# Optimization experiments

Hardware: AMD Instinct MI355X
Metric: run time of the kernel (lower is better)

The kernel has to match this reference:

```python
import jax, jax.numpy as jnp
import numpy as np

BETA = 0.1
CODEBOOK_SIZE = 32768
EMBED_DIM = 4


def setup_inputs() -> dict:
    key = jax.random.key(0)
    kx, ke = jax.random.split(key)
    x = jax.random.normal(kx, (1, 2, EMBED_DIM, 64, 64), dtype=jnp.float32)
    # codebook init mirrors uniform(-1/K, 1/K) but scale doesn't affect correctness;
    # use normal scaled small to keep distances well-conditioned
    E = jax.random.uniform(ke, (CODEBOOK_SIZE, EMBED_DIM), dtype=jnp.float32,
                           minval=-1.0 / CODEBOOK_SIZE, maxval=1.0 / CODEBOOK_SIZE)
    return {"x": x, "E": E}


def reference(x, E):
    b, t, c, h, w = x.shape
    # (B,T,C,H,W) -> (N, C) with N = B*T*H*W
    x_flat = jnp.transpose(x, (0, 1, 3, 4, 2)).reshape(-1, c)
    d = (jnp.sum(x_flat * x_flat, axis=1, keepdims=True)
         + jnp.sum(E * E, axis=1)
         - 2.0 * jnp.einsum('nc,kc->nk', x_flat, E))
    codes = jnp.argmin(d, axis=1)                      # (N,)
    z_q = E[codes].reshape(b, t, h, w, c)              # gather
    z_q = jnp.transpose(z_q, (0, 1, 4, 2, 3))          # (B,T,C,H,W)
    # commitment + codebook loss
    qloss = (jnp.mean((jax.lax.stop_gradient(z_q) - x) ** 2)
             + BETA * jnp.mean((z_q - jax.lax.stop_gradient(x)) ** 2))
    # straight-through estimator
    z_q_st = x + jax.lax.stop_gradient(z_q - x)
    codes = codes.reshape(b, t, h, w)
    return z_q_st, qloss, codes
```

## Files before the change

kernel.cpp:

```cpp
#include <hip/hip_runtime.h>
#include <cfloat>

#define KC    32768
#define NPTS  8192
#define TPB   256
#define PPT   8
#define PTS_PER_BLK (TPB * PPT)
#define NPB   (NPTS / PTS_PER_BLK)
#define NC    256
#define CHUNK (KC / NC)

typedef float v2f __attribute__((ext_vector_type(2)));

__device__ __forceinline__ v2f pk_fma(v2f a, v2f b, v2f c) {
    v2f d; asm("v_pk_fma_f32 %0, %1, %2, %3" : "=v"(d) : "v"(a), "v"(b), "v"(c)); return d;
}
__device__ __forceinline__ v2f pk_add(v2f a, v2f b) {
    v2f d; asm("v_pk_add_f32 %0, %1, %2" : "=v"(d) : "v"(a), "v"(b)); return d;
}
template<int H>
__device__ __forceinline__ v2f pk_mul_s(v2f a, v2f b) {
    v2f d;
    if constexpr (H == 0)
        asm("v_pk_mul_f32 %0, %1, %2 op_sel:[0,0] op_sel_hi:[0,1]" : "=v"(d) : "v"(a), "v"(b));
    else
        asm("v_pk_mul_f32 %0, %1, %2 op_sel:[1,0] op_sel_hi:[1,1]" : "=v"(d) : "v"(a), "v"(b));
    return d;
}
template<int H>
__device__ __forceinline__ v2f pk_fma_s(v2f a, v2f b, v2f c) {
    v2f d;
    if constexpr (H == 0)
        asm("v_pk_fma_f32 %0, %1, %2, %3 op_sel:[0,0,0] op_sel_hi:[0,1,1]" : "=v"(d) : "v"(a), "v"(b), "v"(c));
    else
        asm("v_pk_fma_f32 %0, %1, %2, %3 op_sel:[1,0,0] op_sel_hi:[1,1,1]" : "=v"(d) : "v"(a), "v"(b), "v"(c));
    return d;
}
__device__ __forceinline__ float min3f(float a, float b, float c) {
    float d; asm("v_min3_f32 %0, %1, %2, %3" : "=v"(d) : "v"(a), "v"(b), "v"(c)); return d;
}

__global__ __launch_bounds__(TPB) void k_dist(const float* __restrict__ x,
                                              const float* __restrict__ E,
                                              float* __restrict__ dmn) {
#pragma clang fp contract(off)
    __shared__ __align__(16) float lds[5 * CHUNK];
    float* exL = lds;
    float* eyL = lds + CHUNK;
    float* ezL = lds + 2 * CHUNK;
    float* ewL = lds + 3 * CHUNK;
    float* bL  = lds + 4 * CHUNK;

    const int chunk = blockIdx.x;
    const int pblk  = blockIdx.y;
    const int tid   = threadIdx.x;
    const int kbase = chunk * CHUNK;

    for (int i = tid; i < CHUNK; i += TPB) {
        float4 e = ((const float4*)E)[kbase + i];
        exL[i] = e.x; eyL[i] = e.y; ezL[i] = e.z; ewL[i] = e.w;
        bL[i]  = ((e.x * e.x + e.y * e.y) + e.z * e.z) + e.w * e.w;
    }
    __syncthreads();

    v2f X01[PPT], X23[PPT], Av[PPT];
#pragma unroll
    for (int i = 0; i < PPT; ++i) {
        const int p  = pblk * PTS_PER_BLK + i * TPB + tid;
        const int t  = p >> 12, s = p & 4095;
        const int xb = t * 16384 + s;
        const float x0 = x[xb];
        const float x1 = x[xb + 4096];
        const float x2 = x[xb + 8192];
        const float x3 = x[xb + 12288];
        X01[i] = v2f{x0, x1};
        X23[i] = v2f{x2, x3};
        const float a = ((x0 * x0 + x1 * x1) + x2 * x2) + x3 * x3;
        Av[i] = v2f{a, a};
    }
    const v2f M2 = {-2.0f, -2.0f};

    float bd[PPT];
#pragma unroll
    for (int i = 0; i < PPT; ++i) bd[i] = FLT_MAX;

#pragma unroll 2
    for (int q = 0; q < CHUNK / 4; ++q) {
        float4 vx = *(const float4*)(exL + 4 * q);
        float4 vy = *(const float4*)(eyL + 4 * q);
        float4 vz = *(const float4*)(ezL + 4 * q);
        float4 vw = *(const float4*)(ewL + 4 * q);
        float4 vb = *(const float4*)(bL  + 4 * q);

        const v2f ex0 = {vx.x, vx.y}, ex1 = {vx.z, vx.w};
        const v2f ey0 = {vy.x, vy.y}, ey1 = {vy.z, vy.w};
        const v2f ez0 = {vz.x, vz.y}, ez1 = {vz.z, vz.w};
        const v2f ew0 = {vw.x, vw.y}, ew1 = {vw.z, vw.w};
        const v2f b0  = {vb.x, vb.y}, b1  = {vb.z, vb.w};

#pragma unroll
        for (int i = 0; i < PPT; ++i) {
            v2f m0 = pk_fma_s<1>(X23[i], ew0, pk_fma_s<0>(X23[i], ez0,
                      pk_fma_s<1>(X01[i], ey0, pk_mul_s<0>(X01[i], ex0))));
            v2f m1 = pk_fma_s<1>(X23[i], ew1, pk_fma_s<0>(X23[i], ez1,
                      pk_fma_s<1>(X01[i], ey1, pk_mul_s<0>(X01[i], ex1))));
            v2f d0 = pk_fma(M2, m0, pk_add(Av[i], b0));
            v2f d1 = pk_fma(M2, m1, pk_add(Av[i], b1));
            bd[i] = min3f(min3f(bd[i], d0.x, d0.y), d1.x, d1.y);
        }
    }
#pragma unroll
    for (int i = 0; i < PPT; ++i) {
        const int p = pblk * PTS_PER_BLK + i * TPB + tid;
        dmn[chunk * NPTS + p] = bd[i];
    }
}

__global__ __launch_bounds__(256) void k_merge(const float* __restrict__ x,
                                               const float* __restrict__ E,
                                               const float* __restrict__ dmn,
                                               float* __restrict__ out,
                                               double* __restrict__ partials) {
#pragma clang fp contract(off)
    const int tid  = threadIdx.x;
    const int sub  = tid & 7;
    const int pidx = tid >> 3;
    const int p    = blockIdx.x * 32 + pidx;
    const int t    = p >> 12, s = p & 4095;
    const int xb   = t * 16384 + s;

    const float x0 = x[xb];
    const float x1 = x[xb + 4096];
    const float x2 = x[xb + 8192];
    const float x3 = x[xb + 12288];
    const float a  = ((x0 * x0 + x1 * x1) + x2 * x2) + x3 * x3;

    float bd = FLT_MAX;
    int   bc = 0x7fffffff;
#pragma unroll
    for (int i = 0; i < NC / 8; ++i) {
        const int c = sub + 8 * i;
        float d = dmn[c * NPTS + p];
        if (d < bd) { bd = d; bc = c; }
    }
#pragma unroll
    for (int m = 1; m <= 4; m <<= 1) {
        float d2 = __shfl_xor(bd, m);
        int   c2 = __shfl_xor(bc, m);
        if (d2 < bd || (d2 == bd && c2 < bc)) { bd = d2; bc = c2; }
    }

    const int kb = bc * CHUNK;
    int jloc = 1 << 30;
    for (int jj = 0; jj < 16; ++jj) {
        const int j = sub * 16 + jj;
        float4 e = ((const float4*)E)[kb + j];
        float bn = ((e.x * e.x + e.y * e.y) + e.z * e.z) + e.w * e.w;
        float m_ = __builtin_fmaf(x3, e.w, __builtin_fmaf(x2, e.z,
                    __builtin_fmaf(x1, e.y, x0 * e.x)));
        float t_ = a + bn;
        float d_ = __builtin_fmaf(-2.0f, m_, t_);
        if (d_ == bd) jloc = min(jloc, j);
    }
#pragma unroll
    for (int m = 1; m <= 4; m <<= 1) jloc = min(jloc, __shfl_xor(jloc, m));
    const int bk = kb + (jloc & (CHUNK - 1));

    double ls = 0.0;
    if (sub < 4) {
        const int ch  = sub;
        const int idx = xb + ch * 4096;
        float xv   = x[idx];
        float ev   = E[bk * 4 + ch];
        float diff = ev - xv;
        float sq   = diff * diff;
        out[idx]   = xv + diff;
        ls = (double)sq;
        if (ch == 0) out[32769 + p] = (float)bk;
    }
#pragma unroll
    for (int m = 1; m < 64; m <<= 1) ls += __shfl_xor(ls, m);
    __shared__ double sred[4];
    if ((tid & 63) == 0) sred[tid >> 6] = ls;
    __syncthreads();
    if (tid == 0) partials[blockIdx.x] = sred[0] + sred[1] + sred[2] + sred[3];
}

__global__ void k_loss(const double* __restrict__ partials,
                       float* __restrict__ out) {
#pragma clang fp contract(off)
    if (threadIdx.x == 0 && blockIdx.x == 0) {
        double sum = 0.0;
        for (int i = 0; i < 256; ++i) sum += partials[i];
        float mu = (float)(sum * (1.0 / 32768.0));
        float q  = mu + 0.1f * mu;
        out[32768] = q;
    }
}

extern "C" void kernel_launch(void* const* d_in, const int* in_sizes, int n_in,
                              void* d_out, int out_size, void* d_ws, size_t ws_size,
                              hipStream_t stream) {
    const float* x = (const float*)d_in[0];
    const float* E = (const float*)d_in[1];
    float* out = (float*)d_out;

    char* ws = (char*)d_ws;
    double* partials = (double*)ws;
    float*  dmn      = (float*)(ws + 2048);

    dim3 g(NC, NPB);
    k_dist<<<g, TPB, 0, stream>>>(x, E, dmn);
    k_merge<<<NPTS / 32, 256, 0, stream>>>(x, E, dmn, out, partials);
    k_loss<<<1, 64, 0, stream>>>(partials, out);
}
```

Baseline: 50.31 us.

## Stream codebook via scalar loads from precomputed SoA instead of LDS staging

Adds a prep kernel that writes the codebook as structure-of-arrays with precomputed norms. The distance kernel then reads code pairs through wave-uniform scalar loads used directly as packed-FMA scalar operands, instead of staging the chunk in LDS. Points are packed two per vector lane and pre-scaled by -2. This removes LDS reads and a barrier but adds a launch, and it changes the arithmetic order, so minima may not match the merge kernel's exact recompute.

```diff
diff --git a/kernel.cpp b/kernel.cpp
--- a/kernel.cpp
+++ b/kernel.cpp
@@ -12,107 +12,116 @@
 
 typedef float v2f __attribute__((ext_vector_type(2)));
 
-__device__ __forceinline__ v2f pk_fma(v2f a, v2f b, v2f c) {
-    v2f d; asm("v_pk_fma_f32 %0, %1, %2, %3" : "=v"(d) : "v"(a), "v"(b), "v"(c)); return d;
+template<int H> __device__ __forceinline__ v2f pk_mul_sg(double a, v2f b) {
+    v2f d;
+    if constexpr (H == 0)
+        asm("v_pk_mul_f32 %0, %1, %2 op_sel:[0,0] op_sel_hi:[0,1]" : "=v"(d) : "s"(a), "v"(b));
+    else
+        asm("v_pk_mul_f32 %0, %1, %2 op_sel:[1,0] op_sel_hi:[1,1]" : "=v"(d) : "s"(a), "v"(b));
+    return d;
+}
+template<int H> __device__ __forceinline__ v2f pk_fma_sg(double a, v2f b, v2f c) {
+    v2f d;
+    if constexpr (H == 0)
+        asm("v_pk_fma_f32 %0, %1, %2, %3 op_sel:[0,0,0] op_sel_hi:[0,1,1]" : "=v"(d) : "s"(a), "v"(b), "v"(c));
+    else
+        asm("v_pk_fma_f32 %0, %1, %2, %3 op_sel:[1,0,0] op_sel_hi:[1,1,1]" : "=v"(d) : "s"(a), "v"(b), "v"(c));
+    return d;
+}
+template<int H> __device__ __forceinline__ v2f pk_add_sg(double a, v2f b) {
+    v2f d;
+    if constexpr (H == 0)
+        asm("v_pk_add_f32 %0, %1, %2 op_sel:[0,0] op_sel_hi:[0,1]" : "=v"(d) : "s"(a), "v"(b));
+    else
+        asm("v_pk_add_f32 %0, %1, %2 op_sel:[1,0] op_sel_hi:[1,1]" : "=v"(d) : "s"(a), "v"(b));
+    return d;
 }
 __device__ __forceinline__ v2f pk_add(v2f a, v2f b) {
     v2f d; asm("v_pk_add_f32 %0, %1, %2" : "=v"(d) : "v"(a), "v"(b)); return d;
 }
-template<int H>
-__device__ __forceinline__ v2f pk_mul_s(v2f a, v2f b) {
-    v2f d;
-    if constexpr (H == 0)
-        asm("v_pk_mul_f32 %0, %1, %2 op_sel:[0,0] op_sel_hi:[0,1]" : "=v"(d) : "v"(a), "v"(b));
-    else
-        asm("v_pk_mul_f32 %0, %1, %2 op_sel:[1,0] op_sel_hi:[1,1]" : "=v"(d) : "v"(a), "v"(b));
-    return d;
-}
-template<int H>
-__device__ __forceinline__ v2f pk_fma_s(v2f a, v2f b, v2f c) {
-    v2f d;
-    if constexpr (H == 0)
-        asm("v_pk_fma_f32 %0, %1, %2, %3 op_sel:[0,0,0] op_sel_hi:[0,1,1]" : "=v"(d) : "v"(a), "v"(b), "v"(c));
-    else
-        asm("v_pk_fma_f32 %0, %1, %2, %3 op_sel:[1,0,0] op_sel_hi:[1,1,1]" : "=v"(d) : "v"(a), "v"(b), "v"(c));
-    return d;
-}
 __device__ __forceinline__ float min3f(float a, float b, float c) {
     float d; asm("v_min3_f32 %0, %1, %2, %3" : "=v"(d) : "v"(a), "v"(b), "v"(c)); return d;
 }
 
+__global__ __launch_bounds__(256) void k_prep(const float* __restrict__ E,
+                                              float* __restrict__ ec) {
+#pragma clang fp contract(off)
+    const int k = blockIdx.x * 256 + threadIdx.x;
+    float4 e = ((const float4*)E)[k];
+    ec[k]          = e.x;
+    ec[KC + k]     = e.y;
+    ec[2 * KC + k] = e.z;
+    ec[3 * KC + k] = e.w;
+    ec[4 * KC + k] = ((e.x * e.x + e.y * e.y) + e.z * e.z) + e.w * e.w;
+}
+
 __global__ __launch_bounds__(TPB) void k_dist(const float* __restrict__ x,
-                                              const float* __restrict__ E,
+                                              const float* __restrict__ ec,
                                               float* __restrict__ dmn) {
 #pragma clang fp contract(off)
-    __shared__ __align__(16) float lds[5 * CHUNK];
-    float* exL = lds;
-    float* eyL = lds + CHUNK;
-    float* ezL = lds + 2 * CHUNK;
-    float* ewL = lds + 3 * CHUNK;
-    float* bL  = lds + 4 * CHUNK;
+    const double* E0 = (const double*)(ec);
+    const double* E1 = (const double*)(ec + KC);
+    const double* E2 = (const double*)(ec + 2 * KC);
+    const double* E3 = (const double*)(ec + 3 * KC);
+    const double* Bb = (const double*)(ec + 4 * KC);
 
     const int chunk = blockIdx.x;
     const int pblk  = blockIdx.y;
     const int tid   = threadIdx.x;
-    const int kbase = chunk * CHUNK;
-
-    for (int i = tid; i < CHUNK; i += TPB) {
-        float4 e = ((const float4*)E)[kbase + i];
-        exL[i] = e.x; eyL[i] = e.y; ezL[i] = e.z; ewL[i] = e.w;
-        bL[i]  = ((e.x * e.x + e.y * e.y) + e.z * e.z) + e.w * e.w;
-    }
-    __syncthreads();
-
-    v2f X01[PPT], X23[PPT], Av[PPT];
-#pragma unroll
-    for (int i = 0; i < PPT; ++i) {
-        const int p  = pblk * PTS_PER_BLK + i * TPB + tid;
-        const int t  = p >> 12, s = p & 4095;
-        const int xb = t * 16384 + s;
-        const float x0 = x[xb];
-        const float x1 = x[xb + 4096];
-        const float x2 = x[xb + 8192];
-        const float x3 = x[xb + 12288];
-        X01[i] = v2f{x0, x1};
-        X23[i] = v2f{x2, x3};
-        const float a = ((x0 * x0 + x1 * x1) + x2 * x2) + x3 * x3;
-        Av[i] = v2f{a, a};
-    }
-    const v2f M2 = {-2.0f, -2.0f};
-
-    float bd[PPT];
-#pragma unroll
-    for (int i = 0; i < PPT; ++i) bd[i] = FLT_MAX;
-
-#pragma unroll 2
-    for (int q = 0; q < CHUNK / 4; ++q) {
-        float4 vx = *(const float4*)(exL + 4 * q);
-        float4 vy = *(const float4*)(eyL + 4 * q);
-        float4 vz = *(const float4*)(ezL + 4 * q);
-        float4 vw = *(const float4*)(ewL + 4 * q);
-        float4 vb = *(const float4*)(bL  + 4 * q);
-
-        const v2f ex0 = {vx.x, vx.y}, ex1 = {vx.z, vx.w};
-        const v2f ey0 = {vy.x, vy.y}, ey1 = {vy.z, vy.w};
-        const v2f ez0 = {vz.x, vz.y}, ez1 = {vz.z, vz.w};
-        const v2f ew0 = {vw.x, vw.y}, ew1 = {vw.z, vw.w};
-        const v2f b0  = {vb.x, vb.y}, b1  = {vb.z, vb.w};
-
-#pragma unroll
-        for (int i = 0; i < PPT; ++i) {
-            v2f m0 = pk_fma_s<1>(X23[i], ew0, pk_fma_s<0>(X23[i], ez0,
-                      pk_fma_s<1>(X01[i], ey0, pk_mul_s<0>(X01[i], ex0))));
-            v2f m1 = pk_fma_s<1>(X23[i], ew1, pk_fma_s<0>(X23[i], ez1,
-                      pk_fma_s<1>(X01[i], ey1, pk_mul_s<0>(X01[i], ex1))));
-            v2f d0 = pk_fma(M2, m0, pk_add(Av[i], b0));
-            v2f d1 = pk_fma(M2, m1, pk_add(Av[i], b1));
-            bd[i] = min3f(min3f(bd[i], d0.x, d0.y), d1.x, d1.y);
+    const int kb2   = chunk * (CHUNK / 2);
+
+    v2f Xm0[4], Xm1[4], Xm2[4], Xm3[4], Aab[4];
+#pragma unroll
+    for (int u = 0; u < 4; ++u) {
+        float xs[2][4], aa[2];
+#pragma unroll
+        for (int h = 0; h < 2; ++h) {
+            const int i = 2 * u + h;
+            const int p = pblk * PTS_PER_BLK + i * TPB + tid;
+            const int t = p >> 12, s = p & 4095;
+            const int xb = t * 16384 + s;
+            const float x0 = x[xb], x1 = x[xb + 4096], x2 = x[xb + 8192], x3 = x[xb + 12288];
+            xs[h][0] = x0; xs[h][1] = x1; xs[h][2] = x2; xs[h][3] = x3;
+            aa[h] = ((x0 * x0 + x1 * x1) + x2 * x2) + x3 * x3;
         }
-    }
-#pragma unroll
-    for (int i = 0; i < PPT; ++i) {
-        const int p = pblk * PTS_PER_BLK + i * TPB + tid;
-        dmn[chunk * NPTS + p] = bd[i];
+        Xm0[u] = v2f{-2.0f * xs[0][0], -2.0f * xs[1][0]};
+        Xm1[u] = v2f{-2.0f * xs[0][1], -2.0f * xs[1][1]};
+        Xm2[u] = v2f{-2.0f * xs[0][2], -2.0f * xs[1][2]};
+        Xm3[u] = v2f{-2.0f * xs[0][3], -2.0f * xs[1][3]};
+        Aab[u] = v2f{aa[0], aa[1]};
+    }
+
+    float bdA[4], bdB[4];
+#pragma unroll
+    for (int u = 0; u < 4; ++u) { bdA[u] = FLT_MAX; bdB[u] = FLT_MAX; }
+
+#pragma unroll 4
+    for (int q = 0; q < CHUNK / 2; ++q) {
+        const double se0 = E0[kb2 + q];
+        const double se1 = E1[kb2 + q];
+        const double se2 = E2[kb2 + q];
+        const double se3 = E3[kb2 + q];
+        const double sb  = Bb[kb2 + q];
+#pragma unroll
+        for (int u = 0; u < 4; ++u) {
+            v2f m0 = pk_fma_sg<0>(se3, Xm3[u], pk_fma_sg<0>(se2, Xm2[u],
+                      pk_fma_sg<0>(se1, Xm1[u], pk_mul_sg<0>(se0, Xm0[u]))));
+            v2f t0 = pk_add_sg<0>(sb, Aab[u]);
+            v2f d0 = pk_add(m0, t0);
+            v2f m1 = pk_fma_sg<1>(se3, Xm3[u], pk_fma_sg<1>(se2, Xm2[u],
+                      pk_fma_sg<1>(se1, Xm1[u], pk_mul_sg<1>(se0, Xm0[u]))));
+            v2f t1 = pk_add_sg<1>(sb, Aab[u]);
+            v2f d1 = pk_add(m1, t1);
+            bdA[u] = min3f(bdA[u], d0.x, d1.x);
+            bdB[u] = min3f(bdB[u], d0.y, d1.y);
+        }
+    }
+#pragma unroll
+    for (int u = 0; u < 4; ++u) {
+        const int pA = pblk * PTS_PER_BLK + (2 * u) * TPB + tid;
+        const int pB = pblk * PTS_PER_BLK + (2 * u + 1) * TPB + tid;
+        dmn[chunk * NPTS + pA] = bdA[u];
+        dmn[chunk * NPTS + pB] = bdB[u];
     }
 }
 
@@ -137,7 +146,7 @@
 
     float bd = FLT_MAX;
     int   bc = 0x7fffffff;
-#pragma unroll
+#pragma unroll 8
     for (int i = 0; i < NC / 8; ++i) {
         const int c = sub + 8 * i;
         float d = dmn[c * NPTS + p];
@@ -152,8 +161,8 @@
 
     const int kb = bc * CHUNK;
     int jloc = 1 << 30;
-    for (int jj = 0; jj < 16; ++jj) {
-        const int j = sub * 16 + jj;
+    for (int jj = 0; jj < CHUNK / 8; ++jj) {
+        const int j = sub * (CHUNK / 8) + jj;
         float4 e = ((const float4*)E)[kb + j];
         float bn = ((e.x * e.x + e.y * e.y) + e.z * e.z) + e.w * e.w;
         float m_ = __builtin_fmaf(x3, e.w, __builtin_fmaf(x2, e.z,
@@ -207,10 +216,12 @@
 
     char* ws = (char*)d_ws;
     double* partials = (double*)ws;
-    float*  dmn      = (float*)(ws + 2048);
-
+    float*  ec       = (float*)(ws + 2048);
+    float*  dmn      = (float*)(ws + 2048 + 5 * KC * 4);
+
+    k_prep<<<KC / 256, 256, 0, stream>>>(E, ec);
     dim3 g(NC, NPB);
-    k_dist<<<g, TPB, 0, stream>>>(x, E, dmn);
+    k_dist<<<g, TPB, 0, stream>>>(x, ec, dmn);
     k_merge<<<NPTS / 32, 256, 0, stream>>>(x, E, dmn, out, partials);
     k_loss<<<1, 64, 0, stream>>>(partials, out);
 }
```

New measurement: 55.85 us. +11.0%, slower.
